# Optimization experiments

Hardware: AMD Instinct MI355X
Metric: run time of the kernel (lower is better)

The kernel has to match this reference:

```python
import jax, jax.numpy as jnp
import numpy as np

N, H, V, K = 2048, 1024, 50304, 16
C = V // K  # tokens per POS cluster


def setup_inputs() -> dict:
    key = jax.random.key(0)
    kx, ky, kw, kl = jax.random.split(key, 4)
    x = jax.random.normal(kx, (N, H), dtype=jnp.float32)
    y = jax.random.randint(ky, (N,), 0, V, dtype=jnp.int32)
    # consistent POS label: token y belongs to cluster y // C
    y_pos = (y // C).astype(jnp.int32)
    # pos2token[i] = token ids of cluster i (equal contiguous partition)
    pos2token = jnp.arange(V, dtype=jnp.int32).reshape(K, C)
    # token_in_pos_id[i][v] = within-cluster index of token v in cluster i
    token_in_pos_id = jnp.broadcast_to(jnp.arange(V, dtype=jnp.int32) % C, (K, V))
    cluster_w = jax.random.normal(kw, (H, K), dtype=jnp.float32) * 0.02
    logits = jax.random.normal(kl, (H, V), dtype=jnp.float32) * 0.02
    return {"x": x, "y": y, "y_pos": y_pos, "pos2token": pos2token,
            "token_in_pos_id": token_in_pos_id, "cluster_w": cluster_w, "logits": logits}


def reference(x, y, y_pos, pos2token, token_in_pos_id, cluster_w, logits):
    # cluster (POS) log-probs: [N, K]
    cluster_ll = jax.nn.log_softmax(x @ cluster_w, axis=1)
    # per-cluster weight slices gathered once: [H, K, C]
    W = logits[:, pos2token.reshape(-1)].reshape(H, K, C)
    # tail logits for every token against every cluster's token set: [N, K, C]
    tail_lp = jax.nn.log_softmax(jnp.einsum('nh,hkc->nkc', x, W), axis=-1)
    n = jnp.arange(y.shape[0])
    within = token_in_pos_id[y_pos, y]          # within-cluster target id
    nll = -cluster_ll[n, y_pos] - tail_lp[n, y_pos, within]
    return nll
```

## Files before the change

### kernel.cpp

```cpp
#include <hip/hip_runtime.h>
#include <hip/hip_bf16.h>

#define NROW 2048
#define HDIM 1024
#define VOC  50304
#define KCL  16
#define CDIM 3144

#define MT 128
#define NTC 64
#define NCT ((CDIM + NTC - 1) / NTC)
#define CAP 256

#define WS_SUMEXP 0
#define WS_COUNTS 2048
#define WS_PART   2064
#define WS_ZTGT   4112
#define WS_TCOL   6160
#define WS_ROWS   8208
#define WS_XG     40976

typedef __attribute__((ext_vector_type(8))) short short8;
typedef __attribute__((ext_vector_type(4))) float f32x4;

__device__ __forceinline__ ushort2 f2bf2(float a, float b) {
    union { __hip_bfloat162 h; ushort2 u; } cv;
    cv.h = __float22bfloat162_rn(float2{a, b});
    return cv.u;
}

__global__ void scatter_kernel(const int* __restrict__ y,
                               const int* __restrict__ y_pos,
                               const int* __restrict__ tip,
                               int* ws_i) {
    int n = blockIdx.x * 256 + threadIdx.x;
    if (n >= NROW) return;
    int kn = y_pos[n];
    int slot = atomicAdd(&ws_i[WS_COUNTS + kn], 1);
    ws_i[WS_ROWS + kn * NROW + slot] = n;
    ws_i[WS_TCOL + n] = tip[kn * VOC + y[n]];
}

__global__ void prep_kernel(const float* __restrict__ x,
                            const float* __restrict__ cw,
                            const int* __restrict__ ws_i, float* ws_f) {
    __shared__ __align__(16) short rb[4][128][8];

    const int wv   = threadIdx.x >> 6;
    const int lane = threadIdx.x & 63;
    const int b = blockIdx.x;
    const int k = b >> 6;
    const int slot0 = (b & 63) * 4;
    const int slot  = slot0 + wv;
    const int Mk = ws_i[WS_COUNTS + k];

    float4 v[4];
    if (slot < Mk) {
        const int n = ws_i[WS_ROWS + k * NROW + slot];
        const float4* xr = (const float4*)(x + (size_t)n * HDIM);
#pragma unroll
        for (int q = 0; q < 4; q++) v[q] = xr[q * 64 + lane];
    } else {
#pragma unroll
        for (int q = 0; q < 4; q++) v[q] = float4{0.f, 0.f, 0.f, 0.f};
    }
#pragma unroll
    for (int q = 0; q < 4; q++) {
        union { ushort2 u2[2]; uint2 u; } t;
        t.u2[0] = f2bf2(v[q].x, v[q].y);
        t.u2[1] = f2bf2(v[q].z, v[q].w);
        *(uint2*)&rb[wv][q * 32 + (lane >> 1)][(lane & 1) * 4] = t.u;
    }
    if (slot < Mk) {
        float acc[KCL];
#pragma unroll
        for (int kk = 0; kk < KCL; kk++) acc[kk] = 0.f;
#pragma unroll
        for (int q = 0; q < 4; q++) {
            const float* vf = (const float*)&v[q];
#pragma unroll
            for (int e = 0; e < 4; e++) {
                const int h = q * 256 + lane * 4 + e;
                const float xv = vf[e];
                const float4* cwr = (const float4*)(cw + (size_t)h * KCL);
#pragma unroll
                for (int qq = 0; qq < 4; qq++) {
                    float4 wgt = cwr[qq];
                    acc[qq * 4 + 0] += xv * wgt.x;
                    acc[qq * 4 + 1] += xv * wgt.y;
                    acc[qq * 4 + 2] += xv * wgt.z;
                    acc[qq * 4 + 3] += xv * wgt.w;
                }
            }
        }
#pragma unroll
        for (int off = 32; off >= 1; off >>= 1) {
#pragma unroll
            for (int kk = 0; kk < KCL; kk++) acc[kk] += __shfl_down(acc[kk], off);
        }
        if (lane == 0) {
            const int n = ws_i[WS_ROWS + k * NROW + slot];
            float m = acc[0];
#pragma unroll
            for (int kk = 1; kk < KCL; kk++) m = fmaxf(m, acc[kk]);
            float s = 0.f;
#pragma unroll
            for (int kk = 0; kk < KCL; kk++) s += __expf(acc[kk] - m);
            ws_f[WS_PART + n] = (m + __logf(s)) - acc[k];
        }
    }
    __syncthreads();
    {
        const int h8 = threadIdx.x >> 1;
        const int sp = (threadIdx.x & 1) * 2;
        short* o = (short*)(ws_i + WS_XG)
                 + ((size_t)k * (128 * 256) + (size_t)h8 * 256 + slot0 + sp) * 8;
        *(short8*)(o)     = *(const short8*)&rb[sp][h8][0];
        *(short8*)(o + 8) = *(const short8*)&rb[sp + 1][h8][0];
    }
}

__launch_bounds__(256, 3)
__global__ void tail_kernel(const float* __restrict__ logits,
                            const int* ws_i, float* ws_f) {
    __shared__ int   lrow[MT];
    __shared__ int   ltcol[MT];
    __shared__ float rowsum[MT];

    const int k  = blockIdx.y;
    const int ct = blockIdx.x;
    int Mk = ws_i[WS_COUNTS + k];
    if (Mk > CAP) Mk = CAP;

    const int tid = threadIdx.x;
    const int w  = tid >> 6, l = tid & 63;
    const int wr = (w & 1) * 64;
    const int wc = (w >> 1) * 32;
    const int quad = l >> 4, lm = l & 15;

    const float* bBase0;
    const float* bBase1;
    {
        int c0 = ct * NTC + wc + lm;       if (c0 >= CDIM) c0 = CDIM - 1;
        int c1 = ct * NTC + wc + 16 + lm;  if (c1 >= CDIM) c1 = CDIM - 1;
        const float* base = logits + (size_t)(quad * 8) * VOC + (size_t)k * CDIM;
        bBase0 = base + c0;
        bBase1 = base + c1;
    }
    const short* xgT = (const short*)(ws_i + WS_XG);

    for (int r0 = 0; r0 < Mk; r0 += MT) {
        __syncthreads();
        if (tid < MT) {
            int r = r0 + tid;
            int rid = (r < Mk) ? ws_i[WS_ROWS + k * NROW + r] : -1;
            lrow[tid]  = rid;
            ltcol[tid] = (rid >= 0) ? ws_i[WS_TCOL + rid] : -1;
            rowsum[tid] = 0.f;
        }
        __syncthreads();

        const short* aBase = xgT
            + (((size_t)k * 128 + quad) * 256 + (size_t)(r0 + wr + lm)) * 8;

        f32x4 acc[4][2];
#pragma unroll
        for (int mi = 0; mi < 4; mi++)
#pragma unroll
            for (int ni = 0; ni < 2; ni++) acc[mi][ni] = (f32x4)(0.f);

        float  bv0[2][8], bv1[2][8];
        short8 af0[4],    af1[4];

        auto LOADA = [&](int t, short8* af) {
#pragma unroll
            for (int mi = 0; mi < 4; mi++)
                af[mi] = *(const short8*)(aBase + (size_t)t * 8192 + mi * 128);
        };
        auto LOADB = [&](int t, float bv[2][8]) {
            const float* p0 = bBase0 + (size_t)t * 32 * VOC;
            const float* p1 = bBase1 + (size_t)t * 32 * VOC;
#pragma unroll
            for (int j = 0; j < 8; j++) bv[0][j] = p0[(size_t)j * VOC];
#pragma unroll
            for (int j = 0; j < 8; j++) bv[1][j] = p1[(size_t)j * VOC];
        };
        auto COMPUTE = [&](float bv[2][8], short8* af) {
            short8 bf[2];
#pragma unroll
            for (int ni = 0; ni < 2; ni++) {
                union { ushort2 u2[4]; short8 s8; } u;
#pragma unroll
                for (int jj = 0; jj < 4; jj++)
                    u.u2[jj] = f2bf2(bv[ni][2 * jj], bv[ni][2 * jj + 1]);
                bf[ni] = u.s8;
            }
#pragma unroll
            for (int mi = 0; mi < 4; mi++)
#pragma unroll
                for (int ni = 0; ni < 2; ni++)
                    acc[mi][ni] = __builtin_amdgcn_mfma_f32_16x16x32_bf16(
                        af[mi], bf[ni], acc[mi][ni], 0, 0, 0);
        };

        LOADB(0, bv0);
        LOADA(0, af0);
        for (int t = 0; t < HDIM / 32; t += 2) {
            LOADB(t + 1, bv1);
            LOADA(t + 1, af1);
            COMPUTE(bv0, af0);
            if (t + 2 < HDIM / 32) {
                LOADB(t + 2, bv0);
                LOADA(t + 2, af0);
            }
            COMPUTE(bv1, af1);
        }

#pragma unroll
        for (int mi = 0; mi < 4; mi++) {
#pragma unroll
            for (int r = 0; r < 4; r++) {
                int row_local = wr + mi * 16 + quad * 4 + r;
                int rid = lrow[row_local];
                int tc  = ltcol[row_local];
                float s = 0.f;
#pragma unroll
                for (int ni = 0; ni < 2; ni++) {
                    int cl = ct * NTC + wc + ni * 16 + lm;
                    float z = acc[mi][ni][r];
                    if (rid >= 0 && cl < CDIM) {
                        s += __expf(z);
                        if (cl == tc) ws_f[WS_ZTGT + rid] = z;
                    }
                }
                s += __shfl_xor(s, 1);
                s += __shfl_xor(s, 2);
                s += __shfl_xor(s, 4);
                s += __shfl_xor(s, 8);
                if (lm == 0 && rid >= 0) atomicAdd(&rowsum[row_local], s);
            }
        }
        __syncthreads();
        if (tid < MT) {
            int rid = lrow[tid];
            if (rid >= 0) atomicAdd(&ws_f[WS_SUMEXP + rid], rowsum[tid]);
        }
    }
}

__global__ void finalize_kernel(const float* ws_f, float* __restrict__ out) {
    int n = blockIdx.x * 256 + threadIdx.x;
    if (n >= NROW) return;
    out[n] = ws_f[WS_PART + n] + __logf(ws_f[WS_SUMEXP + n]) - ws_f[WS_ZTGT + n];
}

extern "C" void kernel_launch(void* const* d_in, const int* in_sizes, int n_in,
                              void* d_out, int out_size, void* d_ws, size_t ws_size,
                              hipStream_t stream) {
    const float* x      = (const float*)d_in[0];
    const int*   y      = (const int*)d_in[1];
    const int*   y_pos  = (const int*)d_in[2];
    const int*   tip    = (const int*)d_in[4];
    const float* cw     = (const float*)d_in[5];
    const float* logits = (const float*)d_in[6];
    float* out  = (float*)d_out;
    float* ws_f = (float*)d_ws;
    int*   ws_i = (int*)d_ws;

    hipMemsetAsync(d_ws, 0, (size_t)(NROW + KCL) * 4, stream);

    scatter_kernel<<<NROW / 256, 256, 0, stream>>>(y, y_pos, tip, ws_i);
    prep_kernel<<<KCL * CAP / 4, 256, 0, stream>>>(x, cw, ws_i, ws_f);

    dim3 grid(NCT, KCL);
    tail_kernel<<<grid, 256, 0, stream>>>(logits, ws_i, ws_f);

    finalize_kernel<<<NROW / 256, 256, 0, stream>>>(ws_f, out);
}
```

Baseline: 427.1 us.

## Retile tail GEMM to 192-row by 32-column blocks with swizzled cluster order

The tail kernel now handles one 192-row tile per block instead of looping over 128-row tiles, and uses 32-column tiles instead of 64. The second row tile comes from a grid z dimension and exits early when the cluster has few rows. Block IDs are remapped so neighbouring blocks interleave clusters, and the launch bound asks for 4 blocks per CU. The goal is to read the large fp32 logits slice only once per column tile instead of once per row tile, and to spread work over more blocks. The cost is wasted MFMA work on padded rows when a cluster has far fewer than 192 rows.

```diff
diff --git a/kernel.cpp b/kernel.cpp
--- a/kernel.cpp
+++ b/kernel.cpp
@@ -7,8 +7,8 @@
 #define KCL  16
 #define CDIM 3144
 
-#define MT 128
-#define NTC 64
+#define MT 192
+#define NTC 32
 #define NCT ((CDIM + NTC - 1) / NTC)
 #define CAP 256
 
@@ -120,131 +120,106 @@
     }
 }
 
-__launch_bounds__(256, 3)
+__launch_bounds__(256, 4)
 __global__ void tail_kernel(const float* __restrict__ logits,
                             const int* ws_i, float* ws_f) {
     __shared__ int   lrow[MT];
     __shared__ int   ltcol[MT];
     __shared__ float rowsum[MT];
 
-    const int k  = blockIdx.y;
-    const int ct = blockIdx.x;
+    const int id = blockIdx.x + NCT * blockIdx.y;
+    const int k  = (id & 7) * 2 + ((id >> 3) & 1);
+    const int ct = id >> 4;
+    const int rt = blockIdx.z;
     int Mk = ws_i[WS_COUNTS + k];
     if (Mk > CAP) Mk = CAP;
+    if (rt * MT >= Mk) return;
 
     const int tid = threadIdx.x;
-    const int w  = tid >> 6, l = tid & 63;
-    const int wr = (w & 1) * 64;
-    const int wc = (w >> 1) * 32;
+    if (tid < MT) {
+        int r = rt * MT + tid;
+        int rid = (r < Mk) ? ws_i[WS_ROWS + k * NROW + r] : -1;
+        lrow[tid]  = rid;
+        ltcol[tid] = (rid >= 0) ? ws_i[WS_TCOL + rid] : -1;
+        rowsum[tid] = 0.f;
+    }
+    __syncthreads();
+
+    const int w = tid >> 6, l = tid & 63;
+    const int wr = (w & 1) * 96;
+    const int wc = (w >> 1) * 16;
     const int quad = l >> 4, lm = l & 15;
 
-    const float* bBase0;
-    const float* bBase1;
-    {
-        int c0 = ct * NTC + wc + lm;       if (c0 >= CDIM) c0 = CDIM - 1;
-        int c1 = ct * NTC + wc + 16 + lm;  if (c1 >= CDIM) c1 = CDIM - 1;
-        const float* base = logits + (size_t)(quad * 8) * VOC + (size_t)k * CDIM;
-        bBase0 = base + c0;
-        bBase1 = base + c1;
-    }
     const short* xgT = (const short*)(ws_i + WS_XG);
-
-    for (int r0 = 0; r0 < Mk; r0 += MT) {
-        __syncthreads();
-        if (tid < MT) {
-            int r = r0 + tid;
-            int rid = (r < Mk) ? ws_i[WS_ROWS + k * NROW + r] : -1;
-            lrow[tid]  = rid;
-            ltcol[tid] = (rid >= 0) ? ws_i[WS_TCOL + rid] : -1;
-            rowsum[tid] = 0.f;
-        }
-        __syncthreads();
-
-        const short* aBase = xgT
-            + (((size_t)k * 128 + quad) * 256 + (size_t)(r0 + wr + lm)) * 8;
-
-        f32x4 acc[4][2];
-#pragma unroll
-        for (int mi = 0; mi < 4; mi++)
-#pragma unroll
-            for (int ni = 0; ni < 2; ni++) acc[mi][ni] = (f32x4)(0.f);
-
-        float  bv0[2][8], bv1[2][8];
-        short8 af0[4],    af1[4];
-
-        auto LOADA = [&](int t, short8* af) {
-#pragma unroll
-            for (int mi = 0; mi < 4; mi++)
-                af[mi] = *(const short8*)(aBase + (size_t)t * 8192 + mi * 128);
-        };
-        auto LOADB = [&](int t, float bv[2][8]) {
-            const float* p0 = bBase0 + (size_t)t * 32 * VOC;
-            const float* p1 = bBase1 + (size_t)t * 32 * VOC;
-#pragma unroll
-            for (int j = 0; j < 8; j++) bv[0][j] = p0[(size_t)j * VOC];
-#pragma unroll
-            for (int j = 0; j < 8; j++) bv[1][j] = p1[(size_t)j * VOC];
-        };
-        auto COMPUTE = [&](float bv[2][8], short8* af) {
-            short8 bf[2];
-#pragma unroll
-            for (int ni = 0; ni < 2; ni++) {
-                union { ushort2 u2[4]; short8 s8; } u;
-#pragma unroll
-                for (int jj = 0; jj < 4; jj++)
-                    u.u2[jj] = f2bf2(bv[ni][2 * jj], bv[ni][2 * jj + 1]);
-                bf[ni] = u.s8;
+    const short* aBase = xgT
+        + (((size_t)k * 128 + quad) * 256 + (size_t)(rt * MT + wr + lm)) * 8;
+
+    int c0 = ct * NTC + wc + lm;
+    if (c0 >= CDIM) c0 = CDIM - 1;
+    const float* bBase = logits + (size_t)(quad * 8) * VOC + (size_t)k * CDIM + c0;
+
+    f32x4 acc[6];
+#pragma unroll
+    for (int mi = 0; mi < 6; mi++) acc[mi] = (f32x4)(0.f);
+
+    float  bv0[8], bv1[8];
+    short8 af0[6], af1[6];
+
+    auto LOADB = [&](int t, float* bv) {
+        const float* p = bBase + (size_t)(t * 32) * VOC;
+#pragma unroll
+        for (int j = 0; j < 8; j++) bv[j] = p[(size_t)j * VOC];
+    };
+    auto LOADA = [&](int t, short8* af) {
+        const short* p = aBase + (size_t)t * 8192;
+#pragma unroll
+        for (int mi = 0; mi < 6; mi++)
+            af[mi] = *(const short8*)(p + mi * 128);
+    };
+    auto COMPUTE = [&](float* bv, short8* af) {
+        union { ushort2 u2[4]; short8 s8; } u;
+#pragma unroll
+        for (int jj = 0; jj < 4; jj++) u.u2[jj] = f2bf2(bv[2 * jj], bv[2 * jj + 1]);
+#pragma unroll
+        for (int mi = 0; mi < 6; mi++)
+            acc[mi] = __builtin_amdgcn_mfma_f32_16x16x32_bf16(
+                af[mi], u.s8, acc[mi], 0, 0, 0);
+    };
+
+    LOADB(0, bv0); LOADA(0, af0);
+    LOADB(1, bv1); LOADA(1, af1);
+    for (int t = 0; t < HDIM / 32; t += 2) {
+        COMPUTE(bv0, af0);
+        if (t + 2 < HDIM / 32) { LOADB(t + 2, bv0); LOADA(t + 2, af0); }
+        COMPUTE(bv1, af1);
+        if (t + 3 < HDIM / 32) { LOADB(t + 3, bv1); LOADA(t + 3, af1); }
+    }
+
+    const int cl = ct * NTC + wc + lm;
+#pragma unroll
+    for (int mi = 0; mi < 6; mi++) {
+#pragma unroll
+        for (int r = 0; r < 4; r++) {
+            int row_local = wr + mi * 16 + quad * 4 + r;
+            int rid = lrow[row_local];
+            int tc  = ltcol[row_local];
+            float z = acc[mi][r];
+            float s = 0.f;
+            if (rid >= 0 && cl < CDIM) {
+                s = __expf(z);
+                if (cl == tc) ws_f[WS_ZTGT + rid] = z;
             }
-#pragma unroll
-            for (int mi = 0; mi < 4; mi++)
-#pragma unroll
-                for (int ni = 0; ni < 2; ni++)
-                    acc[mi][ni] = __builtin_amdgcn_mfma_f32_16x16x32_bf16(
-                        af[mi], bf[ni], acc[mi][ni], 0, 0, 0);
-        };
-
-        LOADB(0, bv0);
-        LOADA(0, af0);
-        for (int t = 0; t < HDIM / 32; t += 2) {
-            LOADB(t + 1, bv1);
-            LOADA(t + 1, af1);
-            COMPUTE(bv0, af0);
-            if (t + 2 < HDIM / 32) {
-                LOADB(t + 2, bv0);
-                LOADA(t + 2, af0);
-            }
-            COMPUTE(bv1, af1);
-        }
-
-#pragma unroll
-        for (int mi = 0; mi < 4; mi++) {
-#pragma unroll
-            for (int r = 0; r < 4; r++) {
-                int row_local = wr + mi * 16 + quad * 4 + r;
-                int rid = lrow[row_local];
-                int tc  = ltcol[row_local];
-                float s = 0.f;
-#pragma unroll
-                for (int ni = 0; ni < 2; ni++) {
-                    int cl = ct * NTC + wc + ni * 16 + lm;
-                    float z = acc[mi][ni][r];
-                    if (rid >= 0 && cl < CDIM) {
-                        s += __expf(z);
-                        if (cl == tc) ws_f[WS_ZTGT + rid] = z;
-                    }
-                }
-                s += __shfl_xor(s, 1);
-                s += __shfl_xor(s, 2);
-                s += __shfl_xor(s, 4);
-                s += __shfl_xor(s, 8);
-                if (lm == 0 && rid >= 0) atomicAdd(&rowsum[row_local], s);
-            }
-        }
-        __syncthreads();
-        if (tid < MT) {
-            int rid = lrow[tid];
-            if (rid >= 0) atomicAdd(&ws_f[WS_SUMEXP + rid], rowsum[tid]);
-        }
+            s += __shfl_xor(s, 1);
+            s += __shfl_xor(s, 2);
+            s += __shfl_xor(s, 4);
+            s += __shfl_xor(s, 8);
+            if (lm == 0 && rid >= 0) atomicAdd(&rowsum[row_local], s);
+        }
+    }
+    __syncthreads();
+    if (tid < MT) {
+        int rid = lrow[tid];
+        if (rid >= 0) atomicAdd(&ws_f[WS_SUMEXP + rid], rowsum[tid]);
     }
 }
 
@@ -272,7 +247,7 @@
     scatter_kernel<<<NROW / 256, 256, 0, stream>>>(y, y_pos, tip, ws_i);
     prep_kernel<<<KCL * CAP / 4, 256, 0, stream>>>(x, cw, ws_i, ws_f);
 
-    dim3 grid(NCT, KCL);
+    dim3 grid(NCT, KCL, 2);
     tail_kernel<<<grid, 256, 0, stream>>>(logits, ws_i, ws_f);
 
     finalize_kernel<<<NROW / 256, 256, 0, stream>>>(ws_f, out);
```

After: 420.3 us. No clear change (-1.6%).
